# Kernel optimization log

Measured on AMD Instinct MI355X. Metric: run time of the kernel, lower is better.

The kernel has to match this reference:

```python
import jax, jax.numpy as jnp
import numpy as np

OFFSETS = list(range(0, 8))  # s_prev=0, s_curr=7 -> kernel_size K=8
NEG = -1e9  # finite stand-in for -inf in masked softmax (avoids NaN rows)


def setup_inputs() -> dict:
    key = jax.random.key(0)
    ks = jax.random.split(key, 5)
    B, N, d = 8, 4096, 256
    x = jax.random.normal(ks[0], (B, N, d), dtype=jnp.float32)
    # most-recent-first: index 0 has smallest time delta -> sorted ascending
    delta_times = jnp.sort(jax.random.uniform(ks[1], (B, N), dtype=jnp.float32) * 100.0, axis=1)
    lengths = jax.random.randint(ks[2], (B,), N // 2, N + 1)
    valid_mask = jnp.arange(N)[None, :] < lengths[:, None]  # [B, N] bool
    w = jax.random.normal(ks[3], (len(OFFSETS),), dtype=jnp.float32) * 0.1
    beta = jax.random.normal(ks[4], (1,), dtype=jnp.float32) * 0.1
    return {"x": x, "delta_times": delta_times, "valid_mask": valid_mask, "w": w, "beta": beta}


def _mixer(x, delta_times, valid_mask, w, beta):
    B, N, d = x.shape
    sxs, tds, cvs = [], [], []
    for p in OFFSETS:  # small fixed kernel window, K=8
        if p == 0:
            sxs.append(x)
            tds.append(jnp.zeros((B, N), x.dtype))
            cvs.append(valid_mask)
        else:
            sxs.append(jnp.pad(x[:, p:], ((0, 0), (0, p), (0, 0))))
            tds.append(jnp.pad(jnp.maximum(delta_times[:, p:] - delta_times[:, :N - p], 0.0), ((0, 0), (0, p))))
            cvs.append(jnp.pad(valid_mask[:, p:] & valid_mask[:, :N - p], ((0, 0), (0, p))))
    sx = jnp.stack(sxs, axis=2)  # [B, N, K, d]
    td = jnp.stack(tds, axis=2)  # [B, N, K]
    cv = jnp.stack(cvs, axis=2)  # [B, N, K] bool
    # temporal-decay softmax over offsets (masked positions -> ~0 weight)
    theta = jax.nn.softmax(jnp.where(cv, -td, NEG), axis=2)
    wsm = jax.nn.softmax(w)[None, None, :]  # learnable per-offset weights
    b = jax.nn.sigmoid(beta[0])
    alpha = jnp.where(cv, b * wsm + (1.0 - b) * theta, 0.0)
    alpha = alpha / jnp.maximum(alpha.sum(axis=2, keepdims=True), 1e-8)
    out = jnp.einsum('bnkd,bnk->bnd', sx, alpha)
    return out * valid_mask[..., None].astype(x.dtype)


def reference(x, delta_times, valid_mask, w, beta):
    # Dropout is identity in eval mode.
    return _mixer(x, delta_times, valid_mask, w, beta)
```

## Files before the change

kernel.cpp:

```cpp
#include <hip/hip_runtime.h>


#define NEGV (-1e9f)

constexpr int Bc = 8;
constexpr int Nc = 4096;
constexpr int Dc = 256;
constexpr int Kc = 8;
constexpr int ROWS = 4;

__global__ __launch_bounds__(256) void atm_kernel(
    const float* __restrict__ x,
    const float* __restrict__ dt,
    const void* __restrict__ maskp,
    const float* __restrict__ w,
    const float* __restrict__ beta,
    float* __restrict__ out)
{
    const unsigned char* m8 = (const unsigned char*)maskp;
    const int* m32 = (const int*)maskp;
    const bool is_byte = (m8[1] != 0);

    const int wave = threadIdx.x >> 6;
    const int lane = threadIdx.x & 63;
    const int tiles_per_b = Nc / ROWS;
    const int b = blockIdx.x / tiles_per_b;
    const int tile = blockIdx.x % tiles_per_b;
    const int n = tile * ROWS + wave;
    const long rowm = (long)b * Nc + n;

    float4* __restrict__ out4 = (float4*)out;
    const float4* __restrict__ x4 = (const float4*)x;
    const long o4 = rowm * (Dc / 4) + lane;

    auto getm = [&](long i) -> bool {
        return is_byte ? (m8[i] != 0) : (m32[i] != 0);
    };

    const bool valid_n = getm(rowm);
    if (!valid_n) {
        out4[o4] = make_float4(0.f, 0.f, 0.f, 0.f);
        return;
    }

    float wv[Kc];
    float wmax = -1e30f;
#pragma unroll
    for (int p = 0; p < Kc; ++p) { wv[p] = w[p]; wmax = fmaxf(wmax, wv[p]); }
    float wsum = 0.f;
#pragma unroll
    for (int p = 0; p < Kc; ++p) { wv[p] = expf(wv[p] - wmax); wsum += wv[p]; }
    const float winv = 1.0f / wsum;
    const float bsig = 1.0f / (1.0f + expf(-beta[0]));

    const float dtn = dt[rowm];
    float lg[Kc];
    bool cv[Kc];
    float mx = -1e30f;
#pragma unroll
    for (int p = 0; p < Kc; ++p) {
        const int np = n + p;
        bool c;
        float t = 0.0f;
        if (p == 0) {
            c = true;
        } else if (np < Nc) {
            c = getm(rowm + p);
            t = fmaxf(dt[rowm + p] - dtn, 0.0f);
        } else {
            c = false;
        }
        const float l = c ? -t : NEGV;
        cv[p] = c;
        lg[p] = l;
        mx = fmaxf(mx, l);
    }

    float th[Kc];
    float tsum = 0.f;
#pragma unroll
    for (int p = 0; p < Kc; ++p) { th[p] = expf(lg[p] - mx); tsum += th[p]; }
    const float tinv = 1.0f / tsum;

    float alpha[Kc];
    float asum = 0.f;
#pragma unroll
    for (int p = 0; p < Kc; ++p) {
        const float a = cv[p] ? (bsig * wv[p] * winv + (1.0f - bsig) * th[p] * tinv)
                              : 0.0f;
        alpha[p] = a;
        asum += a;
    }
    const float norm = 1.0f / fmaxf(asum, 1e-8f);

    float4 acc = make_float4(0.f, 0.f, 0.f, 0.f);
#pragma unroll
    for (int p = 0; p < Kc; ++p) {
        if (n + p < Nc) {
            const float a = alpha[p] * norm;
            const float4 xv = x4[o4 + (long)p * (Dc / 4)];
            acc.x = fmaf(a, xv.x, acc.x);
            acc.y = fmaf(a, xv.y, acc.y);
            acc.z = fmaf(a, xv.z, acc.z);
            acc.w = fmaf(a, xv.w, acc.w);
        }
    }
    out4[o4] = acc;
}

extern "C" void kernel_launch(void* const* d_in, const int* in_sizes, int n_in,
                              void* d_out, int out_size, void* d_ws, size_t ws_size,
                              hipStream_t stream) {
    const float* x    = (const float*)d_in[0];
    const float* dt   = (const float*)d_in[1];
    const void*  mask = d_in[2];
    const float* w    = (const float*)d_in[3];
    const float* beta = (const float*)d_in[4];
    float* out = (float*)d_out;

    dim3 grid(Bc * Nc / ROWS);
    dim3 block(256);
    atm_kernel<<<grid, block, 0, stream>>>(x, dt, mask, w, beta, out);
}
```

Measured before the change: 106.9 us.

## Stage x rows in shared memory and compute per-row alphas cooperatively per block

Each block now handles 32 rows. It loads the 39 contiguous x rows needed for the 8-offset window into LDS once, so every x row is read from global memory once per block instead of up to 8 times. Alpha weights are computed by 8 lanes per row using shuffle reductions and stored in shared memory, followed by a barrier. The early exit for invalid rows is removed, so masked rows now load x and compute a zero result. The block also uses about 40KB of LDS, which may limit occupancy.

```diff
diff --git a/kernel.cpp b/kernel.cpp
--- a/kernel.cpp
+++ b/kernel.cpp
@@ -5,9 +5,10 @@
 
 constexpr int Bc = 8;
 constexpr int Nc = 4096;
-constexpr int Dc = 256;
+constexpr int D4 = 64;
 constexpr int Kc = 8;
-constexpr int ROWS = 4;
+constexpr int Tr = 32;
+constexpr int XR = Tr + Kc - 1;
 
 __global__ __launch_bounds__(256) void atm_kernel(
     const float* __restrict__ x,
@@ -17,95 +18,99 @@
     const float* __restrict__ beta,
     float* __restrict__ out)
 {
-    const unsigned char* m8 = (const unsigned char*)maskp;
-    const int* m32 = (const int*)maskp;
-    const bool is_byte = (m8[1] != 0);
+    __shared__ float4 xs[XR * D4];
+    __shared__ float alphas[Tr][Kc];
 
-    const int wave = threadIdx.x >> 6;
-    const int lane = threadIdx.x & 63;
-    const int tiles_per_b = Nc / ROWS;
+    const int tid = threadIdx.x;
+    const int tiles_per_b = Nc / Tr;
     const int b = blockIdx.x / tiles_per_b;
-    const int tile = blockIdx.x % tiles_per_b;
-    const int n = tile * ROWS + wave;
-    const long rowm = (long)b * Nc + n;
+    const int n0 = (blockIdx.x % tiles_per_b) * Tr;
+    const long row0 = (long)b * Nc + n0;
 
-    float4* __restrict__ out4 = (float4*)out;
     const float4* __restrict__ x4 = (const float4*)x;
-    const long o4 = rowm * (Dc / 4) + lane;
-
-    auto getm = [&](long i) -> bool {
-        return is_byte ? (m8[i] != 0) : (m32[i] != 0);
-    };
-
-    const bool valid_n = getm(rowm);
-    if (!valid_n) {
-        out4[o4] = make_float4(0.f, 0.f, 0.f, 0.f);
-        return;
+    const long total4 = (long)Bc * Nc * D4;
+    const long base4 = row0 * D4;
+#pragma unroll
+    for (int i = tid; i < XR * D4; i += 256) {
+        const long g = base4 + i;
+        xs[i] = (g < total4) ? x4[g] : make_float4(0.f, 0.f, 0.f, 0.f);
     }
 
-    float wv[Kc];
-    float wmax = -1e30f;
-#pragma unroll
-    for (int p = 0; p < Kc; ++p) { wv[p] = w[p]; wmax = fmaxf(wmax, wv[p]); }
-    float wsum = 0.f;
-#pragma unroll
-    for (int p = 0; p < Kc; ++p) { wv[p] = expf(wv[p] - wmax); wsum += wv[p]; }
-    const float winv = 1.0f / wsum;
-    const float bsig = 1.0f / (1.0f + expf(-beta[0]));
+    {
+        const int r = tid >> 3;
+        const int p = tid & 7;
+        const int n = n0 + r;
+        const long rowm = row0 + r;
 
-    const float dtn = dt[rowm];
-    float lg[Kc];
-    bool cv[Kc];
-    float mx = -1e30f;
-#pragma unroll
-    for (int p = 0; p < Kc; ++p) {
-        const int np = n + p;
+        const unsigned char* m8 = (const unsigned char*)maskp;
+        const int* m32 = (const int*)maskp;
+        const bool is_byte = (m8[1] != 0);
+        auto getm = [&](long i) -> bool {
+            return is_byte ? (m8[i] != 0) : (m32[i] != 0);
+        };
+
         bool c;
-        float t = 0.0f;
+        float td = 0.f;
         if (p == 0) {
-            c = true;
-        } else if (np < Nc) {
-            c = getm(rowm + p);
-            t = fmaxf(dt[rowm + p] - dtn, 0.0f);
+            c = getm(rowm);
+        } else if (n + p < Nc) {
+            c = getm(rowm) && getm(rowm + p);
+            td = fmaxf(dt[rowm + p] - dt[rowm], 0.f);
         } else {
             c = false;
         }
-        const float l = c ? -t : NEGV;
-        cv[p] = c;
-        lg[p] = l;
-        mx = fmaxf(mx, l);
+        const float lg = c ? -td : NEGV;
+
+        float mx = lg;
+        mx = fmaxf(mx, __shfl_xor(mx, 1));
+        mx = fmaxf(mx, __shfl_xor(mx, 2));
+        mx = fmaxf(mx, __shfl_xor(mx, 4));
+        const float th = expf(lg - mx);
+        float tsum = th;
+        tsum += __shfl_xor(tsum, 1);
+        tsum += __shfl_xor(tsum, 2);
+        tsum += __shfl_xor(tsum, 4);
+
+        const float wv = w[p];
+        float wmax = wv;
+        wmax = fmaxf(wmax, __shfl_xor(wmax, 1));
+        wmax = fmaxf(wmax, __shfl_xor(wmax, 2));
+        wmax = fmaxf(wmax, __shfl_xor(wmax, 4));
+        const float we = expf(wv - wmax);
+        float wsum = we;
+        wsum += __shfl_xor(wsum, 1);
+        wsum += __shfl_xor(wsum, 2);
+        wsum += __shfl_xor(wsum, 4);
+
+        const float bsig = 1.0f / (1.0f + expf(-beta[0]));
+        const float a = c ? (bsig * we / wsum + (1.0f - bsig) * th / tsum) : 0.f;
+        float asum = a;
+        asum += __shfl_xor(asum, 1);
+        asum += __shfl_xor(asum, 2);
+        asum += __shfl_xor(asum, 4);
+        alphas[r][p] = a / fmaxf(asum, 1e-8f);
     }
 
-    float th[Kc];
-    float tsum = 0.f;
+    __syncthreads();
+
+    const int wave = tid >> 6;
+    const int lane = tid & 63;
+    float4* __restrict__ out4 = (float4*)out;
 #pragma unroll
-    for (int p = 0; p < Kc; ++p) { th[p] = expf(lg[p] - mx); tsum += th[p]; }
-    const float tinv = 1.0f / tsum;
-
-    float alpha[Kc];
-    float asum = 0.f;
+    for (int rr = 0; rr < 8; ++rr) {
+        const int r = wave * 8 + rr;
+        float4 acc = make_float4(0.f, 0.f, 0.f, 0.f);
 #pragma unroll
-    for (int p = 0; p < Kc; ++p) {
-        const float a = cv[p] ? (bsig * wv[p] * winv + (1.0f - bsig) * th[p] * tinv)
-                              : 0.0f;
-        alpha[p] = a;
-        asum += a;
-    }
-    const float norm = 1.0f / fmaxf(asum, 1e-8f);
-
-    float4 acc = make_float4(0.f, 0.f, 0.f, 0.f);
-#pragma unroll
-    for (int p = 0; p < Kc; ++p) {
-        if (n + p < Nc) {
-            const float a = alpha[p] * norm;
-            const float4 xv = x4[o4 + (long)p * (Dc / 4)];
+        for (int p = 0; p < Kc; ++p) {
+            const float a = alphas[r][p];
+            const float4 xv = xs[(r + p) * D4 + lane];
             acc.x = fmaf(a, xv.x, acc.x);
             acc.y = fmaf(a, xv.y, acc.y);
             acc.z = fmaf(a, xv.z, acc.z);
             acc.w = fmaf(a, xv.w, acc.w);
         }
+        out4[(row0 + r) * D4 + lane] = acc;
     }
-    out4[o4] = acc;
 }
 
 extern "C" void kernel_launch(void* const* d_in, const int* in_sizes, int n_in,
@@ -118,7 +123,7 @@
     const float* beta = (const float*)d_in[4];
     float* out = (float*)d_out;
 
-    dim3 grid(Bc * Nc / ROWS);
+    dim3 grid(Bc * Nc / Tr);
     dim3 block(256);
     atm_kernel<<<grid, block, 0, stream>>>(x, dt, mask, w, beta, out);
 }
```

Measured after the change: 93.30 us. 12.7% less time.
